# Performance work log

Hardware: AMD Instinct MI355X
Metric: run time of the kernel (lower is better)

The kernel has to match this reference:

```python
import jax, jax.numpy as jnp
import numpy as np

N = 50000          # nodes
E = 600000         # edges
IN, H, HID = 3, 128, 64   # input_size, embed_size, decoder hidden
L = 5              # block_number (GRU layers)
EPS = 1e-12


def _l2norm(v):
    # F.normalize(v, p=2, dim=1)
    return v / jnp.maximum(jnp.linalg.norm(v, axis=1, keepdims=True), EPS)


def setup_inputs() -> dict:
    key = jax.random.key(0)
    ks = jax.random.split(key, 12)
    s = 0.05
    x = jax.random.normal(ks[0], (N, IN), dtype=jnp.float32)
    edge_idx = jax.random.randint(ks[1], (2, E), 0, N, dtype=jnp.int64)
    return {
        "x": x,
        "edge_idx": edge_idx,
        # encoder embed: Linear(IN, H)
        "W_embed": jax.random.normal(ks[2], (H, IN), dtype=jnp.float32) * s,
        "b_embed": jnp.zeros((H,), dtype=jnp.float32),
        # L stacked GRU(H, H) params, torch gate order (r, z, n)
        "w_ih": jax.random.normal(ks[3], (L, 3 * H, H), dtype=jnp.float32) * s,
        "w_hh": jax.random.normal(ks[4], (L, 3 * H, H), dtype=jnp.float32) * s,
        "b_ih": jax.random.normal(ks[5], (L, 3 * H), dtype=jnp.float32) * s,
        "b_hh": jax.random.normal(ks[6], (L, 3 * H), dtype=jnp.float32) * s,
        # decoder: Linear(H, HID) -> ReLU -> Linear(HID, 1)
        "W_hid": jax.random.normal(ks[7], (HID, H), dtype=jnp.float32) * s,
        "b_hid": jnp.zeros((HID,), dtype=jnp.float32),
        "W_out": jax.random.normal(ks[8], (1, HID), dtype=jnp.float32) * s,
        "b_out": jnp.zeros((1,), dtype=jnp.float32),
    }


def reference(x, edge_idx, W_embed, b_embed, w_ih, w_hh, b_ih, b_hh,
              W_hid, b_hid, W_out, b_out):
    row, col = edge_idx[0], edge_idx[1]
    n = x.shape[0]

    # symmetric degree normalization (deg + 1)^-0.5, identical every layer
    deg = jnp.zeros((n,), dtype=x.dtype).at[col].add(1.0) + 1.0
    dinv = deg ** -0.5
    norm = dinv[row] * dinv[col]            # [E]

    h0 = _l2norm(jax.nn.relu(x @ W_embed.T + b_embed))  # [N, H]

    def step(h, params):
        wih, whh, bih, bhh = params
        # message + add-aggregate: out[col] += norm * h[row]
        msg = norm[:, None] * h[row]                     # [E, H]
        agg = jax.ops.segment_sum(msg, col, num_segments=n)  # [N, H]
        # GRU step: input = agg, hidden = h (torch gate order r, z, n)
        gi = agg @ wih.T + bih                           # [N, 3H]
        gh = h @ whh.T + bhh                             # [N, 3H]
        i_r, i_z, i_n = jnp.split(gi, 3, axis=1)
        h_r, h_z, h_n = jnp.split(gh, 3, axis=1)
        r = jax.nn.sigmoid(i_r + h_r)
        zg = jax.nn.sigmoid(i_z + h_z)
        ng = jnp.tanh(i_n + r * h_n)
        hn = _l2norm((1.0 - zg) * ng + zg * h)
        return hn, hn

    _, hs = jax.lax.scan(step, h0, (w_ih, w_hh, b_ih, b_hh))  # hs: [L, N, H]
    all_h = jnp.concatenate([h0[None], hs], axis=0)           # [L+1, N, H]
    z = jnp.max(all_h, axis=0)                                # layer-wise max-pool

    z = jax.nn.relu(z @ W_hid.T + b_hid)
    return z @ W_out.T + b_out                                # [N, 1]
```

## Files before the change

### kernel.cpp

```cpp
#include <hip/hip_runtime.h>
#include <math.h>


#define NTHREADS 256
#define SCAN_CHUNK 1024

typedef __attribute__((ext_vector_type(8))) short s16x8;
typedef __attribute__((ext_vector_type(4))) float f32x4;

union U8 { s16x8 v; ushort4 h[2]; int4 q; };

__device__ __forceinline__ unsigned short f2bf(float f) {
  union { float f; unsigned u; } x; x.f = f;
  unsigned u = x.u + 0x7FFFu + ((x.u >> 16) & 1u);
  return (unsigned short)(u >> 16);
}
__device__ __forceinline__ float bf2f(unsigned short s) {
  union { unsigned u; float f; } x; x.u = ((unsigned)s) << 16;
  return x.f;
}


__global__ void count_deg(const int* __restrict__ col, int* deg, int E) {
  int e = blockIdx.x * NTHREADS + threadIdx.x;
  if (e < E) atomicAdd(&deg[col[e]], 1);
}

__global__ void block_reduce(const int* __restrict__ cnt, int* __restrict__ bsum,
                             float* __restrict__ dinv, int n) {
  __shared__ int red[NTHREADS];
  int b = blockIdx.x, t = threadIdx.x;
  int base = b * SCAN_CHUNK + t * 4;
  int s = 0;
#pragma unroll
  for (int i = 0; i < 4; ++i) {
    int idx = base + i;
    if (idx < n) {
      int c = cnt[idx];
      s += c;
      dinv[idx] = rsqrtf((float)c + 1.0f);
    }
  }
  red[t] = s;
  __syncthreads();
  for (int off = NTHREADS / 2; off > 0; off >>= 1) {
    if (t < off) red[t] += red[t + off];
    __syncthreads();
  }
  if (t == 0) bsum[b] = red[0];
}

__global__ void scan_partials(const int* __restrict__ bsum, int* __restrict__ boff,
                              int* __restrict__ row_ptr_n, int nb) {
  int t = threadIdx.x;
  int s = (t < nb) ? bsum[t] : 0;
  int orig = s;
#pragma unroll
  for (int off = 1; off < 64; off <<= 1) {
    int v = __shfl_up(s, off);
    if (t >= off) s += v;
  }
  if (t < nb) boff[t] = s - orig;
  if (t == nb - 1) *row_ptr_n = s;
}

__global__ void scan_final(const int* __restrict__ cnt, const int* __restrict__ boff,
                           int* __restrict__ row_ptr, int* __restrict__ cursor, int n) {
  __shared__ int sums[NTHREADS];
  int b = blockIdx.x, t = threadIdx.x;
  int base = b * SCAN_CHUNK + t * 4;
  int v[4];
  int s = 0;
#pragma unroll
  for (int i = 0; i < 4; ++i) { int idx = base + i; v[i] = (idx < n) ? cnt[idx] : 0; s += v[i]; }
  sums[t] = s;
  __syncthreads();
  for (int off = 1; off < NTHREADS; off <<= 1) {
    int a = (t >= off) ? sums[t - off] : 0;
    __syncthreads();
    sums[t] += a;
    __syncthreads();
  }
  int run = boff[b] + sums[t] - s;
#pragma unroll
  for (int i = 0; i < 4; ++i) {
    int idx = base + i;
    if (idx < n) { row_ptr[idx] = run; cursor[idx] = run; }
    run += v[i];
  }
}

__global__ void scatter_edges(const int* __restrict__ row, const int* __restrict__ col,
                              int* cursor, int* __restrict__ src, int E) {
  int e = blockIdx.x * NTHREADS + threadIdx.x;
  if (e >= E) return;
  int r = row[e], c = col[e];
  int p = atomicAdd(&cursor[c], 1);
  src[p] = r;
}


__global__ void pack_weights(const float* __restrict__ w_ih, const float* __restrict__ w_hh,
                             unsigned short* __restrict__ out) {
  int idx = blockIdx.x * NTHREADS + threadIdx.x;
  if (idx >= 491520) return;
  int e = idx & 7;
  int lane = (idx >> 3) & 63;
  int ft = (idx >> 9) & 7;
  int v = idx >> 12;
  int g = v % 6;
  int u = v / 6;
  int ks = u & 3;
  int layer = u >> 2;
  int k = 32 * ks + (e & 3) + 4 * ((lane >> 4) & 3) + 16 * (e >> 2);
  int j = 16 * ft + (lane & 15);
  const float* src = (g < 3) ? w_ih : w_hh;
  int gate = g % 3;
  float val = src[(size_t)layer * 49152 + (size_t)(gate * 128 + j) * 128 + k];
  out[idx] = f2bf(val);
}

__global__ void pack_whid(const float* __restrict__ W_hid, unsigned short* __restrict__ out) {
  int idx = blockIdx.x * NTHREADS + threadIdx.x;
  if (idx >= 8192) return;
  int e = idx & 7;
  int lane = (idx >> 3) & 63;
  int ft = (idx >> 9) & 3;
  int ks = idx >> 11;
  int k = 32 * ks + (e & 3) + 4 * ((lane >> 4) & 3) + 16 * (e >> 2);
  int j = 16 * ft + (lane & 15);
  out[idx] = f2bf(W_hid[j * 128 + k]);
}


__global__ void encoder(const float* __restrict__ x, const float* __restrict__ W,
                        const float* __restrict__ b, unsigned short* __restrict__ hb, int n) {
  int node = blockIdx.x * 4 + (threadIdx.x >> 6);
  int lane = threadIdx.x & 63;
  if (node >= n) return;
  float x0 = x[node * 3 + 0], x1 = x[node * 3 + 1], x2 = x[node * 3 + 2];
  int j0 = lane, j1 = lane + 64;
  float v0 = fmaxf(fmaf(W[j0 * 3 + 2], x2, fmaf(W[j0 * 3 + 1], x1, fmaf(W[j0 * 3], x0, b[j0]))), 0.f);
  float v1 = fmaxf(fmaf(W[j1 * 3 + 2], x2, fmaf(W[j1 * 3 + 1], x1, fmaf(W[j1 * 3], x0, b[j1]))), 0.f);
  float ss = v0 * v0 + v1 * v1;
#pragma unroll
  for (int sh = 32; sh > 0; sh >>= 1) ss += __shfl_down(ss, sh);
  ss = __shfl(ss, 0);
  float sc = 1.0f / fmaxf(sqrtf(ss), 1e-12f);
  size_t base = (size_t)node * 128;
  hb[base + j0] = f2bf(v0 * sc);
  hb[base + j1] = f2bf(v1 * sc);
}


__global__ void aggregate(const int* __restrict__ row_ptr, const int* __restrict__ src,
                          const float* __restrict__ dinv, const unsigned short* __restrict__ hb,
                          unsigned short* __restrict__ aggb, int n) {
  int node = blockIdx.x * 4 + (threadIdx.x >> 6);
  int lane = threadIdx.x & 63;
  if (node >= n) return;
  const unsigned* hw = (const unsigned*)hb;
  int pb = row_ptr[node], pe = row_ptr[node + 1];
  float aL[4] = {0.f, 0.f, 0.f, 0.f};
  float aH[4] = {0.f, 0.f, 0.f, 0.f};
  int p = pb;
  for (; p + 8 <= pe; p += 8) {
    int s[8]; unsigned u[8]; float w[8];
#pragma unroll
    for (int i = 0; i < 8; ++i) s[i] = src[p + i];
#pragma unroll
    for (int i = 0; i < 8; ++i) {
      w[i] = dinv[s[i]];
      u[i] = hw[(size_t)s[i] * 64 + lane];
    }
#pragma unroll
    for (int i = 0; i < 8; ++i) {
      aL[i & 3] = fmaf(w[i], bf2f((unsigned short)(u[i] & 0xFFFFu)), aL[i & 3]);
      aH[i & 3] = fmaf(w[i], bf2f((unsigned short)(u[i] >> 16)), aH[i & 3]);
    }
  }
  if (p + 4 <= pe) {
    int s[4]; unsigned u[4]; float w[4];
#pragma unroll
    for (int i = 0; i < 4; ++i) s[i] = src[p + i];
#pragma unroll
    for (int i = 0; i < 4; ++i) {
      w[i] = dinv[s[i]];
      u[i] = hw[(size_t)s[i] * 64 + lane];
    }
#pragma unroll
    for (int i = 0; i < 4; ++i) {
      aL[i] = fmaf(w[i], bf2f((unsigned short)(u[i] & 0xFFFFu)), aL[i]);
      aH[i] = fmaf(w[i], bf2f((unsigned short)(u[i] >> 16)), aH[i]);
    }
    p += 4;
  }
  for (; p < pe; ++p) {
    int s = src[p];
    float w = dinv[s];
    unsigned u = hw[(size_t)s * 64 + lane];
    aL[0] = fmaf(w, bf2f((unsigned short)(u & 0xFFFFu)), aL[0]);
    aH[0] = fmaf(w, bf2f((unsigned short)(u >> 16)), aH[0]);
  }
  float dc = dinv[node];
  float a0 = ((aL[0] + aL[1]) + (aL[2] + aL[3])) * dc;
  float a1 = ((aH[0] + aH[1]) + (aH[2] + aH[3])) * dc;
  unsigned o = ((unsigned)f2bf(a1) << 16) | (unsigned)f2bf(a0);
  ((unsigned*)(aggb + (size_t)node * 128))[lane] = o;
}


__global__ __launch_bounds__(1024) void gru_mfma(
    const unsigned short* __restrict__ aggb, const unsigned short* __restrict__ hbc,
    unsigned short* __restrict__ hbn,
    const int4* __restrict__ wpk, const float* __restrict__ bih,
    const float* __restrict__ bhh, int n) {
  __shared__ unsigned short aggS[64 * 132];
  __shared__ unsigned short hS[64 * 132];
  __shared__ float partS[64 * 8];
  __shared__ float scv[64];
  int tid = threadIdx.x;
  int base = blockIdx.x * 64;
  int w = tid >> 6, l = tid & 63;
  int mh = w & 1, fh = w >> 1;
  int lr = l & 15, lg = l >> 4;
  int jj = fh * 16 + lr;

#pragma unroll
  for (int rep = 0; rep < 2; ++rep) {
    int idx = tid + rep * 1024;
    int row = idx >> 5, c4 = idx & 31;
    int gr = base + row; if (gr > n - 1) gr = n - 1;
    ushort4 ua = *(const ushort4*)(aggb + (size_t)gr * 128 + c4 * 4);
    ushort4 uh = *(const ushort4*)(hbc + (size_t)gr * 128 + c4 * 4);
    *(ushort4*)&aggS[row * 132 + c4 * 4] = ua;
    *(ushort4*)&hS[row * 132 + c4 * 4] = uh;
  }
  __syncthreads();

  f32x4 acc[2][6];
#pragma unroll
  for (int mt = 0; mt < 2; ++mt)
#pragma unroll
    for (int g = 0; g < 6; ++g) { acc[mt][g][0] = 0.f; acc[mt][g][1] = 0.f; acc[mt][g][2] = 0.f; acc[mt][g][3] = 0.f; }

#pragma unroll
  for (int ks = 0; ks < 4; ++ks) {
    U8 fa[2], fhh[2];
#pragma unroll
    for (int mt = 0; mt < 2; ++mt) {
      int boff = (mh * 32 + mt * 16 + lr) * 132 + ks * 32 + lg * 4;
      fa[mt].h[0] = *(const ushort4*)&aggS[boff];
      fa[mt].h[1] = *(const ushort4*)&aggS[boff + 16];
      fhh[mt].h[0] = *(const ushort4*)&hS[boff];
      fhh[mt].h[1] = *(const ushort4*)&hS[boff + 16];
    }
#pragma unroll
    for (int g = 0; g < 6; ++g) {
      U8 bw; bw.q = wpk[((ks * 6 + g) * 8 + fh) * 64 + l];
      const U8& a0 = (g < 3) ? fa[0] : fhh[0];
      const U8& a1 = (g < 3) ? fa[1] : fhh[1];
      acc[0][g] = __builtin_amdgcn_mfma_f32_16x16x32_bf16(a0.v, bw.v, acc[0][g], 0, 0, 0);
      acc[1][g] = __builtin_amdgcn_mfma_f32_16x16x32_bf16(a1.v, bw.v, acc[1][g], 0, 0, 0);
    }
  }

  float br = bih[jj], bz = bih[128 + jj], bn = bih[256 + jj];
  float cr = bhh[jj], cz = bhh[128 + jj], cn = bhh[256 + jj];
  float hn_out[2][4];
#pragma unroll
  for (int mt = 0; mt < 2; ++mt)
#pragma unroll
    for (int e = 0; e < 4; ++e) {
      int row = mh * 32 + mt * 16 + lg * 4 + e;
      float ir = acc[mt][0][e], iz = acc[mt][1][e], inn = acc[mt][2][e];
      float hr = acc[mt][3][e], hz = acc[mt][4][e], hnv = acc[mt][5][e];
      float r = 1.f / (1.f + __expf(-(ir + hr + br + cr)));
      float z = 1.f / (1.f + __expf(-(iz + hz + bz + cz)));
      float ng = tanhf(inn + bn + r * (hnv + cn));
      float hv = bf2f(hS[row * 132 + jj]);
      float hn = (1.f - z) * ng + z * hv;
      hn_out[mt][e] = hn;
      float p = hn * hn;
      p += __shfl_xor(p, 1);
      p += __shfl_xor(p, 2);
      p += __shfl_xor(p, 4);
      p += __shfl_xor(p, 8);
      if (lr == 0) partS[row * 8 + fh] = p;
    }
  __syncthreads();
  if (tid < 64) {
    float ss = 0.f;
#pragma unroll
    for (int f = 0; f < 8; ++f) ss += partS[tid * 8 + f];
    scv[tid] = 1.f / fmaxf(sqrtf(ss), 1e-12f);
  }
  __syncthreads();

#pragma unroll
  for (int mt = 0; mt < 2; ++mt)
#pragma unroll
    for (int e = 0; e < 4; ++e) {
      int row = mh * 32 + mt * 16 + lg * 4 + e;
      aggS[row * 132 + jj] = f2bf(hn_out[mt][e] * scv[row]);
    }
  __syncthreads();

#pragma unroll
  for (int rep = 0; rep < 2; ++rep) {
    int idx = tid + rep * 1024;
    int row = idx >> 5, c4 = idx & 31;
    int gr = base + row;
    if (gr < n) {
      ushort4 hv4 = *(const ushort4*)&aggS[row * 132 + c4 * 4];
      *(ushort4*)(hbn + (size_t)gr * 128 + c4 * 4) = hv4;
    }
  }
}


__global__ __launch_bounds__(1024) void gru_dec(
    const unsigned short* __restrict__ aggb, const unsigned short* __restrict__ hbc,
    const unsigned short* __restrict__ h0, const unsigned short* __restrict__ h1,
    const unsigned short* __restrict__ h2, const unsigned short* __restrict__ h3,
    const int4* __restrict__ wpk, const float* __restrict__ bih,
    const float* __restrict__ bhh,
    const int4* __restrict__ wdpk, const float* __restrict__ bh,
    const float* __restrict__ Wo, const float* __restrict__ bo,
    float* __restrict__ out, int n) {
  __shared__ unsigned short aggS[64 * 132];
  __shared__ unsigned short hS[64 * 132];
  __shared__ float partS[64 * 8];
  __shared__ float scv[64];
  int tid = threadIdx.x;
  int base = blockIdx.x * 64;
  int w = tid >> 6, l = tid & 63;
  int mh = w & 1, fh = w >> 1;
  int lr = l & 15, lg = l >> 4;
  int jj = fh * 16 + lr;

#pragma unroll
  for (int rep = 0; rep < 2; ++rep) {
    int idx = tid + rep * 1024;
    int row = idx >> 5, c4 = idx & 31;
    int gr = base + row; if (gr > n - 1) gr = n - 1;
    ushort4 ua = *(const ushort4*)(aggb + (size_t)gr * 128 + c4 * 4);
    ushort4 uh = *(const ushort4*)(hbc + (size_t)gr * 128 + c4 * 4);
    *(ushort4*)&aggS[row * 132 + c4 * 4] = ua;
    *(ushort4*)&hS[row * 132 + c4 * 4] = uh;
  }
  __syncthreads();

  f32x4 acc[2][6];
#pragma unroll
  for (int mt = 0; mt < 2; ++mt)
#pragma unroll
    for (int g = 0; g < 6; ++g) { acc[mt][g][0] = 0.f; acc[mt][g][1] = 0.f; acc[mt][g][2] = 0.f; acc[mt][g][3] = 0.f; }

#pragma unroll
  for (int ks = 0; ks < 4; ++ks) {
    U8 fa[2], fhh[2];
#pragma unroll
    for (int mt = 0; mt < 2; ++mt) {
      int boff = (mh * 32 + mt * 16 + lr) * 132 + ks * 32 + lg * 4;
      fa[mt].h[0] = *(const ushort4*)&aggS[boff];
      fa[mt].h[1] = *(const ushort4*)&aggS[boff + 16];
      fhh[mt].h[0] = *(const ushort4*)&hS[boff];
      fhh[mt].h[1] = *(const ushort4*)&hS[boff + 16];
    }
#pragma unroll
    for (int g = 0; g < 6; ++g) {
      U8 bw; bw.q = wpk[((ks * 6 + g) * 8 + fh) * 64 + l];
      const U8& a0 = (g < 3) ? fa[0] : fhh[0];
      const U8& a1 = (g < 3) ? fa[1] : fhh[1];
      acc[0][g] = __builtin_amdgcn_mfma_f32_16x16x32_bf16(a0.v, bw.v, acc[0][g], 0, 0, 0);
      acc[1][g] = __builtin_amdgcn_mfma_f32_16x16x32_bf16(a1.v, bw.v, acc[1][g], 0, 0, 0);
    }
  }

  float br = bih[jj], bz = bih[128 + jj], bn = bih[256 + jj];
  float cr = bhh[jj], cz = bhh[128 + jj], cn = bhh[256 + jj];
  float hn_out[2][4];
#pragma unroll
  for (int mt = 0; mt < 2; ++mt)
#pragma unroll
    for (int e = 0; e < 4; ++e) {
      int row = mh * 32 + mt * 16 + lg * 4 + e;
      float ir = acc[mt][0][e], iz = acc[mt][1][e], inn = acc[mt][2][e];
      float hr = acc[mt][3][e], hz = acc[mt][4][e], hnv = acc[mt][5][e];
      float r = 1.f / (1.f + __expf(-(ir + hr + br + cr)));
      float z = 1.f / (1.f + __expf(-(iz + hz + bz + cz)));
      float ng = tanhf(inn + bn + r * (hnv + cn));
      float hv = bf2f(hS[row * 132 + jj]);
      float hn = (1.f - z) * ng + z * hv;
      hn_out[mt][e] = hn;
      float p = hn * hn;
      p += __shfl_xor(p, 1);
      p += __shfl_xor(p, 2);
      p += __shfl_xor(p, 4);
      p += __shfl_xor(p, 8);
      if (lr == 0) partS[row * 8 + fh] = p;
    }
  __syncthreads();
  if (tid < 64) {
    float ss = 0.f;
#pragma unroll
    for (int f = 0; f < 8; ++f) ss += partS[tid * 8 + f];
    scv[tid] = 1.f / fmaxf(sqrtf(ss), 1e-12f);
  }
  __syncthreads();

#pragma unroll
  for (int mt = 0; mt < 2; ++mt)
#pragma unroll
    for (int e = 0; e < 4; ++e) {
      int row = mh * 32 + mt * 16 + lg * 4 + e;
      aggS[row * 132 + jj] = f2bf(hn_out[mt][e] * scv[row]);
    }
  __syncthreads();

  const unsigned short* hp[4] = {h0, h1, h2, h3};
#pragma unroll
  for (int rep = 0; rep < 2; ++rep) {
    int idx = tid + rep * 1024;
    int row = idx >> 5, c4 = idx & 31;
    int gr = base + row; if (gr > n - 1) gr = n - 1;
    size_t o = (size_t)gr * 128 + c4 * 4;
    ushort4 m = *(const ushort4*)&aggS[row * 132 + c4 * 4];
    ushort4 u4 = *(const ushort4*)&hS[row * 132 + c4 * 4];
    m.x = (bf2f(u4.x) > bf2f(m.x)) ? u4.x : m.x;
    m.y = (bf2f(u4.y) > bf2f(m.y)) ? u4.y : m.y;
    m.z = (bf2f(u4.z) > bf2f(m.z)) ? u4.z : m.z;
    m.w = (bf2f(u4.w) > bf2f(m.w)) ? u4.w : m.w;
#pragma unroll
    for (int li = 0; li < 4; ++li) {
      ushort4 uu = *(const ushort4*)(hp[li] + o);
      m.x = (bf2f(uu.x) > bf2f(m.x)) ? uu.x : m.x;
      m.y = (bf2f(uu.y) > bf2f(m.y)) ? uu.y : m.y;
      m.z = (bf2f(uu.z) > bf2f(m.z)) ? uu.z : m.z;
      m.w = (bf2f(uu.w) > bf2f(m.w)) ? uu.w : m.w;
    }
    *(ushort4*)&hS[row * 132 + c4 * 4] = m;
  }
  __syncthreads();

  int mq = w & 3, fq = w >> 2;
  f32x4 dacc;
  dacc[0] = 0.f; dacc[1] = 0.f; dacc[2] = 0.f; dacc[3] = 0.f;
#pragma unroll
  for (int ks = 0; ks < 4; ++ks) {
    U8 fz;
    int boff = (mq * 16 + lr) * 132 + ks * 32 + lg * 4;
    fz.h[0] = *(const ushort4*)&hS[boff];
    fz.h[1] = *(const ushort4*)&hS[boff + 16];
    U8 bw; bw.q = wdpk[(ks * 4 + fq) * 64 + l];
    dacc = __builtin_amdgcn_mfma_f32_16x16x32_bf16(fz.v, bw.v, dacc, 0, 0, 0);
  }
  int j = fq * 16 + lr;
  float bj = bh[j], wj = Wo[j];
#pragma unroll
  for (int e = 0; e < 4; ++e) {
    float v = fmaxf(dacc[e] + bj, 0.f) * wj;
    v += __shfl_xor(v, 1);
    v += __shfl_xor(v, 2);
    v += __shfl_xor(v, 4);
    v += __shfl_xor(v, 8);
    if (lr == 0) partS[(mq * 16 + lg * 4 + e) * 4 + fq] = v;
  }
  __syncthreads();
  if (tid < 64) {
    int gr = base + tid;
    if (gr < n) {
      float o4 = (partS[tid * 4 + 0] + partS[tid * 4 + 1]) +
                 (partS[tid * 4 + 2] + partS[tid * 4 + 3]);
      out[gr] = o4 + bo[0];
    }
  }
}


extern "C" void kernel_launch(void* const* d_in, const int* in_sizes, int n_in,
                              void* d_out, int out_size, void* d_ws, size_t ws_size,
                              hipStream_t stream) {
  const float* x       = (const float*)d_in[0];
  const int*   edge    = (const int*)d_in[1];
  const float* W_embed = (const float*)d_in[2];
  const float* b_embed = (const float*)d_in[3];
  const float* w_ih    = (const float*)d_in[4];
  const float* w_hh    = (const float*)d_in[5];
  const float* b_ih    = (const float*)d_in[6];
  const float* b_hh    = (const float*)d_in[7];
  const float* W_hid   = (const float*)d_in[8];
  const float* b_hid   = (const float*)d_in[9];
  const float* W_out   = (const float*)d_in[10];
  const float* b_out   = (const float*)d_in[11];
  float* out = (float*)d_out;

  const int N = in_sizes[0] / 3;
  const int E = in_sizes[1] / 2;
  const int NB = (N + SCAN_CHUNK - 1) / SCAN_CHUNK;

  char* ws = (char*)d_ws;
  size_t off = 0;
  auto alloc = [&](size_t bytes) -> void* {
    void* p = ws + off;
    off = (off + bytes + 511) & ~(size_t)511;
    return p;
  };
  int*   deg     = (int*)alloc((size_t)N * 4);
  float* dinv    = (float*)alloc((size_t)N * 4);
  int*   row_ptr = (int*)alloc((size_t)(N + 1) * 4);
  int*   cursor  = (int*)alloc((size_t)N * 4);
  int*   bsum    = (int*)alloc((size_t)NB * 4);
  int*   boff    = (int*)alloc((size_t)NB * 4);
  int*   srcv    = (int*)alloc((size_t)E * 4);
  unsigned short* wpack  = (unsigned short*)alloc((size_t)491520 * 2);
  unsigned short* wdpack = (unsigned short*)alloc((size_t)8192 * 2);
  unsigned short* aggb   = (unsigned short*)alloc((size_t)N * 128 * 2);
  unsigned short* hbs[5];
  for (int i = 0; i < 5; ++i) hbs[i] = (unsigned short*)alloc((size_t)N * 128 * 2);

  const int* erow = edge;
  const int* ecol = edge + E;

  hipMemsetAsync(deg, 0, (size_t)N * 4, stream);
  count_deg<<<(E + NTHREADS - 1) / NTHREADS, NTHREADS, 0, stream>>>(ecol, deg, E);
  block_reduce<<<NB, NTHREADS, 0, stream>>>(deg, bsum, dinv, N);
  scan_partials<<<1, 64, 0, stream>>>(bsum, boff, row_ptr + N, NB);
  scan_final<<<NB, NTHREADS, 0, stream>>>(deg, boff, row_ptr, cursor, N);
  scatter_edges<<<(E + NTHREADS - 1) / NTHREADS, NTHREADS, 0, stream>>>(erow, ecol, cursor, srcv, E);

  pack_weights<<<(491520 + NTHREADS - 1) / NTHREADS, NTHREADS, 0, stream>>>(w_ih, w_hh, wpack);
  pack_whid<<<32, NTHREADS, 0, stream>>>(W_hid, wdpack);

  encoder<<<(N + 3) / 4, NTHREADS, 0, stream>>>(x, W_embed, b_embed, hbs[0], N);

  for (int l = 0; l < 4; ++l) {
    aggregate<<<(N + 3) / 4, NTHREADS, 0, stream>>>(row_ptr, srcv, dinv, hbs[l], aggb, N);
    gru_mfma<<<(N + 63) / 64, 1024, 0, stream>>>(
        aggb, hbs[l], hbs[l + 1],
        (const int4*)(wpack + (size_t)l * 98304),
        b_ih + (size_t)l * 384, b_hh + (size_t)l * 384, N);
  }

  aggregate<<<(N + 3) / 4, NTHREADS, 0, stream>>>(row_ptr, srcv, dinv, hbs[4], aggb, N);
  gru_dec<<<(N + 63) / 64, 1024, 0, stream>>>(
      aggb, hbs[4], hbs[0], hbs[1], hbs[2], hbs[3],
      (const int4*)(wpack + (size_t)4 * 98304),
      b_ih + (size_t)4 * 384, b_hh + (size_t)4 * 384,
      (const int4*)wdpack, b_hid, W_out, b_out, out, N);
}
```

Baseline: 428.5 us.

## Store node features in feature-chunked layout so aggregation gathers stay cache-resident

After: 610.4 us. 1.42x slower.

```diff
diff --git a/kernel.cpp b/kernel.cpp
--- a/kernel.cpp
+++ b/kernel.cpp
@@ -147,71 +147,69 @@
   for (int sh = 32; sh > 0; sh >>= 1) ss += __shfl_down(ss, sh);
   ss = __shfl(ss, 0);
   float sc = 1.0f / fmaxf(sqrtf(ss), 1e-12f);
-  size_t base = (size_t)node * 128;
-  hb[base + j0] = f2bf(v0 * sc);
-  hb[base + j1] = f2bf(v1 * sc);
-}
-
-
-__global__ void aggregate(const int* __restrict__ row_ptr, const int* __restrict__ src,
-                          const float* __restrict__ dinv, const unsigned short* __restrict__ hb,
-                          unsigned short* __restrict__ aggb, int n) {
-  int node = blockIdx.x * 4 + (threadIdx.x >> 6);
-  int lane = threadIdx.x & 63;
+  size_t o0 = ((size_t)(j0 >> 5) * n + node) * 32 + (j0 & 31);
+  size_t o1 = ((size_t)(j1 >> 5) * n + node) * 32 + (j1 & 31);
+  hb[o0] = f2bf(v0 * sc);
+  hb[o1] = f2bf(v1 * sc);
+}
+
+
+__global__ __launch_bounds__(256) void aggregate(
+    const int* __restrict__ row_ptr, const int* __restrict__ srcv,
+    const float* __restrict__ dinv, const unsigned short* __restrict__ hc,
+    unsigned short* __restrict__ aggc, int n) {
+  int b = blockIdx.x;
+  int r = b & 7, g = b >> 3;
+  int chunk = r >> 1;
+  int sub = g * 2 + (r & 1);
+  int node = sub * 4 + (threadIdx.x >> 6);
   if (node >= n) return;
-  const unsigned* hw = (const unsigned*)hb;
+  int l = threadIdx.x & 63;
+  int e = l >> 4, f2 = l & 15;
+  const unsigned* hw = (const unsigned*)hc + (size_t)chunk * n * 16;
   int pb = row_ptr[node], pe = row_ptr[node + 1];
-  float aL[4] = {0.f, 0.f, 0.f, 0.f};
-  float aH[4] = {0.f, 0.f, 0.f, 0.f};
+  float a0A = 0.f, a1A = 0.f, a0B = 0.f, a1B = 0.f;
   int p = pb;
   for (; p + 8 <= pe; p += 8) {
-    int s[8]; unsigned u[8]; float w[8];
-#pragma unroll
-    for (int i = 0; i < 8; ++i) s[i] = src[p + i];
-#pragma unroll
-    for (int i = 0; i < 8; ++i) {
-      w[i] = dinv[s[i]];
-      u[i] = hw[(size_t)s[i] * 64 + lane];
-    }
-#pragma unroll
-    for (int i = 0; i < 8; ++i) {
-      aL[i & 3] = fmaf(w[i], bf2f((unsigned short)(u[i] & 0xFFFFu)), aL[i & 3]);
-      aH[i & 3] = fmaf(w[i], bf2f((unsigned short)(u[i] >> 16)), aH[i & 3]);
-    }
-  }
-  if (p + 4 <= pe) {
-    int s[4]; unsigned u[4]; float w[4];
-#pragma unroll
-    for (int i = 0; i < 4; ++i) s[i] = src[p + i];
-#pragma unroll
-    for (int i = 0; i < 4; ++i) {
-      w[i] = dinv[s[i]];
-      u[i] = hw[(size_t)s[i] * 64 + lane];
-    }
-#pragma unroll
-    for (int i = 0; i < 4; ++i) {
-      aL[i] = fmaf(w[i], bf2f((unsigned short)(u[i] & 0xFFFFu)), aL[i]);
-      aH[i] = fmaf(w[i], bf2f((unsigned short)(u[i] >> 16)), aH[i]);
-    }
-    p += 4;
-  }
-  for (; p < pe; ++p) {
-    int s = src[p];
-    float w = dinv[s];
-    unsigned u = hw[(size_t)s * 64 + lane];
-    aL[0] = fmaf(w, bf2f((unsigned short)(u & 0xFFFFu)), aL[0]);
-    aH[0] = fmaf(w, bf2f((unsigned short)(u >> 16)), aH[0]);
-  }
-  float dc = dinv[node];
-  float a0 = ((aL[0] + aL[1]) + (aL[2] + aL[3])) * dc;
-  float a1 = ((aH[0] + aH[1]) + (aH[2] + aH[3])) * dc;
-  unsigned o = ((unsigned)f2bf(a1) << 16) | (unsigned)f2bf(a0);
-  ((unsigned*)(aggb + (size_t)node * 128))[lane] = o;
+    int sA = srcv[p + e];
+    int sB = srcv[p + 4 + e];
+    float wA = dinv[sA], wB = dinv[sB];
+    unsigned uA = hw[(size_t)sA * 16 + f2];
+    unsigned uB = hw[(size_t)sB * 16 + f2];
+    a0A = fmaf(wA, bf2f((unsigned short)(uA & 0xFFFFu)), a0A);
+    a1A = fmaf(wA, bf2f((unsigned short)(uA >> 16)), a1A);
+    a0B = fmaf(wB, bf2f((unsigned short)(uB & 0xFFFFu)), a0B);
+    a1B = fmaf(wB, bf2f((unsigned short)(uB >> 16)), a1B);
+  }
+  if (p < pe) {
+    int q = p + e;
+    int s = (q < pe) ? srcv[q] : srcv[pb];
+    float w = (q < pe) ? dinv[s] : 0.f;
+    unsigned u = hw[(size_t)s * 16 + f2];
+    a0A = fmaf(w, bf2f((unsigned short)(u & 0xFFFFu)), a0A);
+    a1A = fmaf(w, bf2f((unsigned short)(u >> 16)), a1A);
+    if (p + 4 < pe) {
+      int q2 = q + 4;
+      int s2 = (q2 < pe) ? srcv[q2] : srcv[pb];
+      float w2 = (q2 < pe) ? dinv[s2] : 0.f;
+      unsigned u2 = hw[(size_t)s2 * 16 + f2];
+      a0B = fmaf(w2, bf2f((unsigned short)(u2 & 0xFFFFu)), a0B);
+      a1B = fmaf(w2, bf2f((unsigned short)(u2 >> 16)), a1B);
+    }
+  }
+  float a0 = a0A + a0B, a1 = a1A + a1B;
+  a0 += __shfl_xor(a0, 16); a0 += __shfl_xor(a0, 32);
+  a1 += __shfl_xor(a1, 16); a1 += __shfl_xor(a1, 32);
+  if (e == 0) {
+    float dc = dinv[node];
+    unsigned o = ((unsigned)f2bf(a1 * dc) << 16) | (unsigned)f2bf(a0 * dc);
+    ((unsigned*)aggc)[(size_t)chunk * n * 16 + (size_t)node * 16 + f2] = o;
+  }
 }
 
 
 __global__ __launch_bounds__(1024) void gru_mfma(
-    const unsigned short* __restrict__ aggb, const unsigned short* __restrict__ hbc,
+    const unsigned short* __restrict__ aggc, const unsigned short* __restrict__ hbc,
     unsigned short* __restrict__ hbn,
     const int4* __restrict__ wpk, const float* __restrict__ bih,
     const float* __restrict__ bhh, int n) {
@@ -231,8 +229,9 @@
     int idx = tid + rep * 1024;
     int row = idx >> 5, c4 = idx & 31;
     int gr = base + row; if (gr > n - 1) gr = n - 1;
-    ushort4 ua = *(const ushort4*)(aggb + (size_t)gr * 128 + c4 * 4);
-    ushort4 uh = *(const ushort4*)(hbc + (size_t)gr * 128 + c4 * 4);
+    size_t off = ((size_t)(c4 >> 3) * n + gr) * 32 + (c4 & 7) * 4;
+    ushort4 ua = *(const ushort4*)(aggc + off);
+    ushort4 uh = *(const ushort4*)(hbc + off);
     *(ushort4*)&aggS[row * 132 + c4 * 4] = ua;
     *(ushort4*)&hS[row * 132 + c4 * 4] = uh;
   }
@@ -313,14 +312,15 @@
     int gr = base + row;
     if (gr < n) {
       ushort4 hv4 = *(const ushort4*)&aggS[row * 132 + c4 * 4];
-      *(ushort4*)(hbn + (size_t)gr * 128 + c4 * 4) = hv4;
+      size_t off = ((size_t)(c4 >> 3) * n + gr) * 32 + (c4 & 7) * 4;
+      *(ushort4*)(hbn + off) = hv4;
     }
   }
 }
 
 
 __global__ __launch_bounds__(1024) void gru_dec(
-    const unsigned short* __restrict__ aggb, const unsigned short* __restrict__ hbc,
+    const unsigned short* __restrict__ aggc, const unsigned short* __restrict__ hbc,
     const unsigned short* __restrict__ h0, const unsigned short* __restrict__ h1,
     const unsigned short* __restrict__ h2, const unsigned short* __restrict__ h3,
     const int4* __restrict__ wpk, const float* __restrict__ bih,
@@ -344,8 +344,9 @@
     int idx = tid + rep * 1024;
     int row = idx >> 5, c4 = idx & 31;
     int gr = base + row; if (gr > n - 1) gr = n - 1;
-    ushort4 ua = *(const ushort4*)(aggb + (size_t)gr * 128 + c4 * 4);
-    ushort4 uh = *(const ushort4*)(hbc + (size_t)gr * 128 + c4 * 4);
+    size_t off = ((size_t)(c4 >> 3) * n + gr) * 32 + (c4 & 7) * 4;
+    ushort4 ua = *(const ushort4*)(aggc + off);
+    ushort4 uh = *(const ushort4*)(hbc + off);
     *(ushort4*)&aggS[row * 132 + c4 * 4] = ua;
     *(ushort4*)&hS[row * 132 + c4 * 4] = uh;
   }
@@ -425,7 +426,7 @@
     int idx = tid + rep * 1024;
     int row = idx >> 5, c4 = idx & 31;
     int gr = base + row; if (gr > n - 1) gr = n - 1;
-    size_t o = (size_t)gr * 128 + c4 * 4;
+    size_t o = ((size_t)(c4 >> 3) * n + gr) * 32 + (c4 & 7) * 4;
     ushort4 m = *(const ushort4*)&aggS[row * 132 + c4 * 4];
     ushort4 u4 = *(const ushort4*)&hS[row * 132 + c4 * 4];
     m.x = (bf2f(u4.x) > bf2f(m.x)) ? u4.x : m.x;
@@ -499,6 +500,8 @@
   const int N = in_sizes[0] / 3;
   const int E = in_sizes[1] / 2;
   const int NB = (N + SCAN_CHUNK - 1) / SCAN_CHUNK;
+  const int G4 = (N + 3) / 4;
+  const int gridA = ((G4 + 1) / 2) * 8;
 
   char* ws = (char*)d_ws;
   size_t off = 0;
@@ -536,14 +539,14 @@
   encoder<<<(N + 3) / 4, NTHREADS, 0, stream>>>(x, W_embed, b_embed, hbs[0], N);
 
   for (int l = 0; l < 4; ++l) {
-    aggregate<<<(N + 3) / 4, NTHREADS, 0, stream>>>(row_ptr, srcv, dinv, hbs[l], aggb, N);
+    aggregate<<<gridA, NTHREADS, 0, stream>>>(row_ptr, srcv, dinv, hbs[l], aggb, N);
     gru_mfma<<<(N + 63) / 64, 1024, 0, stream>>>(
         aggb, hbs[l], hbs[l + 1],
         (const int4*)(wpack + (size_t)l * 98304),
         b_ih + (size_t)l * 384, b_hh + (size_t)l * 384, N);
   }
 
-  aggregate<<<(N + 3) / 4, NTHREADS, 0, stream>>>(row_ptr, srcv, dinv, hbs[4], aggb, N);
+  aggregate<<<gridA, NTHREADS, 0, stream>>>(row_ptr, srcv, dinv, hbs[4], aggb, N);
   gru_dec<<<(N + 63) / 64, 1024, 0, stream>>>(
       aggb, hbs[4], hbs[0], hbs[1], hbs[2], hbs[3],
       (const int4*)(wpack + (size_t)4 * 98304),
```
